# Optimization experiments

Hardware: AMD Instinct MI355X
Metric: run time of the kernel (lower is better)

## Reference

```python
import jax, jax.numpy as jnp
import numpy as np

D_MODEL = 1024
N_HEADS = 16
HEAD_DIM = D_MODEL // N_HEADS
NUM_MEM = 32
D_FF = 4 * D_MODEL
EPS = 1e-5


def _layer_norm(x, g, b):
    mu = jnp.mean(x, axis=-1, keepdims=True)
    var = jnp.mean(jnp.square(x - mu), axis=-1, keepdims=True)
    return (x - mu) * jax.lax.rsqrt(var + EPS) * g + b


def setup_inputs() -> dict:
    key = jax.random.key(0)
    ks = jax.random.split(key, 16)
    E, F, M = D_MODEL, D_FF, NUM_MEM
    s = 1.0 / np.sqrt(E)
    inp = {
        "src": jax.random.normal(ks[0], (2048, 2, E), dtype=jnp.float32),
        "in_proj_w": jax.random.uniform(ks[1], (3 * E, E), jnp.float32, -s, s),
        "in_proj_b": jnp.zeros((3 * E,), jnp.float32),
        "out_w": jax.random.uniform(ks[2], (E, E), jnp.float32, -s, s),
        "out_b": jnp.zeros((E,), jnp.float32),
        "mem_k": jax.random.normal(ks[3], (M, 1, E), jnp.float32) * (1.0 / HEAD_DIM),
        "mem_v": jax.random.normal(ks[4], (M, 1, E), jnp.float32) * (1.0 / M),
        "w1": jax.random.uniform(ks[5], (F, E), jnp.float32, -s, s),
        "b1": jnp.zeros((F,), jnp.float32),
        "w2": jax.random.uniform(ks[6], (E, F), jnp.float32, -1.0 / np.sqrt(F), 1.0 / np.sqrt(F)),
        "b2": jnp.zeros((E,), jnp.float32),
        "ln1_g": jnp.ones((E,), jnp.float32),
        "ln1_b": jnp.zeros((E,), jnp.float32),
        "ln2_g": jnp.ones((E,), jnp.float32),
        "ln2_b": jnp.zeros((E,), jnp.float32),
    }
    return inp


def reference(src, in_proj_w, in_proj_b, out_w, out_b, mem_k, mem_v,
              w1, b1, w2, b2, ln1_g, ln1_b, ln2_g, ln2_b):
    T, B, E = src.shape
    H, d, M = N_HEADS, HEAD_DIM, NUM_MEM

    # --- self-attention with learned memory k/v tokens (dropout=0, eval) ---
    qkv = src @ in_proj_w.T + in_proj_b          # [T, B, 3E]
    q, k, v = jnp.split(qkv, 3, axis=-1)
    q = q * (d ** -0.5)

    # scaled memory tokens appended to K/V along the sequence axis
    mk = (d ** 0.5) * jnp.broadcast_to(mem_k, (M, B, E))
    mv = (M ** 0.5) * jnp.broadcast_to(mem_v, (M, B, E))
    k = jnp.concatenate([k, mk], axis=0)          # [T+M, B, E]
    v = jnp.concatenate([v, mv], axis=0)

    qh = q.reshape(T, B, H, d)
    kh = k.reshape(T + M, B, H, d)
    vh = v.reshape(T + M, B, H, d)

    scores = jnp.einsum('tbhd,sbhd->bhts', qh, kh)  # [B, H, T, T+M]
    attn = jax.nn.softmax(scores, axis=-1)
    ctx = jnp.einsum('bhts,sbhd->tbhd', attn, vh).reshape(T, B, E)
    attn_out = ctx @ out_w.T + out_b

    # --- residual + LN, FFN, residual + LN (post-norm, relu) ---
    x = _layer_norm(src + attn_out, ln1_g, ln1_b)
    ffn = jax.nn.relu(x @ w1.T + b1) @ w2.T + b2
    return _layer_norm(x + ffn, ln2_g, ln2_b)
```

## Files before the change

### kernel.cpp

```cpp
#include <hip/hip_runtime.h>
#include <hip/hip_bf16.h>
#include <cstdint>


using bf16 = __hip_bfloat16;
typedef __attribute__((ext_vector_type(8))) __bf16 bf16x8;
typedef __attribute__((ext_vector_type(4))) __bf16 bf16x4;
typedef __attribute__((ext_vector_type(4))) float f32x4;

__device__ __forceinline__ void gload_lds16(const void* g, void* l) {
    auto gp = (const __attribute__((address_space(1))) void*)(uintptr_t)g;
    auto lp = (__attribute__((address_space(3))) void*)(uint32_t)(uintptr_t)l;
    __builtin_amdgcn_global_load_lds(gp, lp, 16, 0, 0);
}

__device__ __forceinline__ float fast_exp2(float x) {
#if __has_builtin(__builtin_amdgcn_exp2f)
    return __builtin_amdgcn_exp2f(x);
#else
    float r;
    asm("v_exp_f32 %0, %1" : "=v"(r) : "v"(x));
    return r;
#endif
}

__device__ __forceinline__ bf16 bf16_rn(float x) {
    uint32_t u = __builtin_bit_cast(uint32_t, x);
    uint16_t h = (uint16_t)((u + 0x8000u) >> 16);
    return __builtin_bit_cast(bf16, h);
}

__device__ __forceinline__ float bf2f(__bf16 x) {
    return (float)x;
}

template <int EPI>
__global__ __launch_bounds__(256, 2) void gemm_bt(
    const bf16* __restrict__ A, const bf16* __restrict__ B,
    const float* __restrict__ bias, bf16* __restrict__ Cb,
    int M, int N, int K, int lda) {
    __shared__ alignas(16) bf16 As[128 * 32];
    __shared__ alignas(16) bf16 Bs[128 * 32];

    const int tid = threadIdx.x;
    const int wid = tid >> 6;
    const int lane = tid & 63;
    const int g = lane >> 4;
    const int li = lane & 15;

    if (EPI == 3) {
        const int zo = blockIdx.z * K;
        A += zo;
        B += zo;
    }

    int wg = blockIdx.y * gridDim.x + blockIdx.x;
    const int nwg = gridDim.x * gridDim.y;
    const int cpx = nwg >> 3;
    wg = (wg & 7) * cpx + (wg >> 3);
    const int bx = wg % (int)gridDim.x;
    const int by = wg / (int)gridDim.x;

    const int row0 = by * 128;
    const int col0 = bx * 128;
    const int wr = (wid >> 1) * 64;
    const int wc = (wid & 1) * 64;

    const int c0 = wid, c1 = wid + 4;
    const int srow = lane >> 2;
    const int scol = (lane & 3) * 8;

    const bf16* Ag0 = A + (size_t)(row0 + c0 * 16 + srow) * lda + scol;
    const bf16* Ag1 = A + (size_t)(row0 + c1 * 16 + srow) * lda + scol;
    const bf16* Bg0 = B + (size_t)(col0 + c0 * 16 + srow) * lda + scol;
    const bf16* Bg1 = B + (size_t)(col0 + c1 * 16 + srow) * lda + scol;

    bf16* lA0 = &As[c0 * 512];
    bf16* lA1 = &As[c1 * 512];
    bf16* lB0 = &Bs[c0 * 512];
    bf16* lB1 = &Bs[c1 * 512];

    f32x4 acc[4][4];
#pragma unroll
    for (int i = 0; i < 4; ++i)
#pragma unroll
        for (int j = 0; j < 4; ++j) acc[i][j] = (f32x4){0.f, 0.f, 0.f, 0.f};

    for (int k0 = 0; k0 < K; k0 += 32) {
        gload_lds16(Ag0 + k0, lA0);
        gload_lds16(Ag1 + k0, lA1);
        gload_lds16(Bg0 + k0, lB0);
        gload_lds16(Bg1 + k0, lB1);
        __syncthreads();

        bf16x8 af[4], bfr[4];
#pragma unroll
        for (int i = 0; i < 4; ++i) {
            af[i] = *(const bf16x8*)&As[(wr + i * 16 + li) * 32 + g * 8];
            bfr[i] = *(const bf16x8*)&Bs[(wc + i * 16 + li) * 32 + g * 8];
        }
#pragma unroll
        for (int i = 0; i < 4; ++i)
#pragma unroll
            for (int j = 0; j < 4; ++j)
                acc[i][j] = __builtin_amdgcn_mfma_f32_16x16x32_bf16(af[i], bfr[j], acc[i][j], 0, 0, 0);
        __syncthreads();
    }

#pragma unroll
    for (int i = 0; i < 4; ++i) {
#pragma unroll
        for (int j = 0; j < 4; ++j) {
            const int col = col0 + wc + j * 16 + li;
            const float bv = (EPI == 3 && blockIdx.z != 0) ? 0.f : bias[col];
#pragma unroll
            for (int r = 0; r < 4; ++r) {
                const int row = row0 + wr + i * 16 + g * 4 + r;
                const size_t idx = (size_t)row * N + col;
                float v = acc[i][j][r] + bv;
                if (EPI == 0) {
                    if (col < 1024) v *= 0.18033688011112042f;
                    Cb[idx] = bf16_rn(v);
                } else if (EPI == 2) {
                    Cb[idx] = bf16_rn(v > 0.f ? v : 0.f);
                } else {
                    Cb[(size_t)blockIdx.z * ((size_t)M * N) + idx] = bf16_rn(v);
                }
            }
        }
    }
}

__global__ __launch_bounds__(256) void transpose_v(const bf16* __restrict__ qkv,
                                                   const bf16* __restrict__ mv,
                                                   bf16* __restrict__ vt) {
    __shared__ bf16 tile[64][72];
    const int t = blockIdx.x;
    const int h = blockIdx.y;
    const int b = blockIdx.z;
    const int tid = threadIdx.x;
    const int r = tid >> 2;
    const int c = (tid & 3) * 16;
    const int s0 = t * 64;
    if (t < 32) {
        const bf16* p = qkv + (size_t)((s0 + r) * 2 + b) * 3072 + 2048 + h * 64 + c;
        *(bf16x8*)&tile[r][c] = *(const bf16x8*)p;
        *(bf16x8*)&tile[r][c + 8] = *(const bf16x8*)(p + 8);
    } else if (r < 32) {
        const bf16* p = mv + (size_t)r * 1024 + h * 64 + c;
        *(bf16x8*)&tile[r][c] = *(const bf16x8*)p;
        *(bf16x8*)&tile[r][c + 8] = *(const bf16x8*)(p + 8);
    }
    __syncthreads();
    const int d = tid >> 2;
    const int sc = (tid & 3) * 16;
    const int smax = (t < 32) ? 64 : 32;
    if (sc < smax) {
        bf16 tmp[16];
#pragma unroll
        for (int j = 0; j < 16; ++j) tmp[j] = tile[sc + j][d];
        bf16* q = vt + (size_t)((b * 16 + h) * 64 + d) * 2080 + s0 + sc;
        *(bf16x8*)q = *(const bf16x8*)&tmp[0];
        *(bf16x8*)(q + 8) = *(const bf16x8*)&tmp[8];
    }
}

__global__ __launch_bounds__(256, 2) void attn_kernel(
    const bf16* __restrict__ qkv, const bf16* __restrict__ mk,
    const bf16* __restrict__ vt, bf16* __restrict__ ctx) {
    __shared__ alignas(16) bf16 Kst[4][64 * 64];
    __shared__ alignas(16) bf16 Vst[4][64 * 64];
    __shared__ alignas(16) bf16 Plds[4][32 * 64];

    const int tid = threadIdx.x;
    const int wid = tid >> 6;
    const int lane = tid & 63;
    const int g = lane >> 4;
    const int li = lane & 15;

    const int h = blockIdx.x;
    const int b = blockIdx.z;
    const int q0 = blockIdx.y * 128 + wid * 32;

    bf16* pl = &Plds[wid][0];
    const bf16* vth = vt + (size_t)((b * 16 + h) * 64) * 2080;

    const int srow8 = lane >> 3;
    const int sslot = (lane & 7) ^ srow8;

#define STAGE_KV(buf, t)                                                                       \
    {                                                                                          \
        const int _s0 = (t) * 64;                                                              \
        _Pragma("unroll") for (int j = 0; j < 2; ++j) {                                        \
            const int rw = (wid * 2 + j) * 8 + srow8;                                          \
            gload_lds16(qkv + (size_t)((_s0 + rw) * 2 + b) * 3072 + 1024 + h * 64 + sslot * 8, \
                        &Kst[buf][(wid * 2 + j) * 512]);                                       \
            gload_lds16(vth + (size_t)rw * 2080 + _s0 + sslot * 8,                             \
                        &Vst[buf][(wid * 2 + j) * 512]);                                       \
        }                                                                                      \
    }

    bf16x8 qf[2][2];
#pragma unroll
    for (int mi = 0; mi < 2; ++mi)
#pragma unroll
        for (int kd = 0; kd < 2; ++kd)
            qf[mi][kd] = *(const bf16x8*)(qkv + (size_t)((q0 + mi * 16 + li) * 2 + b) * 3072 +
                                          h * 64 + kd * 32 + g * 8);

    f32x4 o[2][4];
    float lrow[2][4];
#pragma unroll
    for (int mi = 0; mi < 2; ++mi) {
#pragma unroll
        for (int ni = 0; ni < 4; ++ni) o[mi][ni] = (f32x4){0.f, 0.f, 0.f, 0.f};
#pragma unroll
        for (int r = 0; r < 4; ++r) lrow[mi][r] = 0.f;
    }

    STAGE_KV(0, 0);
    STAGE_KV(1, 1);

    for (int tp = 0; tp < 16; ++tp) {
        const int t0 = tp * 2;
        __syncthreads();
        if (t0 + 2 < 32) STAGE_KV((t0 + 2) & 3, t0 + 2);
        if (t0 + 3 < 32) STAGE_KV((t0 + 3) & 3, t0 + 3);

#pragma unroll
        for (int ti = 0; ti < 2; ++ti) {
            const int t = t0 + ti;
            const int cur = t & 3;

            bf16x8 kf[4][2];
#pragma unroll
            for (int si = 0; si < 4; ++si)
#pragma unroll
                for (int kd = 0; kd < 2; ++kd)
                    kf[si][kd] = *(const bf16x8*)&Kst[cur][(si * 16 + li) * 64 +
                                                           (((kd * 4 + g) ^ (li & 7)) * 8)];

            f32x4 sa[2][4];
#pragma unroll
            for (int mi = 0; mi < 2; ++mi)
#pragma unroll
                for (int si = 0; si < 4; ++si) sa[mi][si] = (f32x4){0.f, 0.f, 0.f, 0.f};
            __builtin_amdgcn_s_setprio(1);
#pragma unroll
            for (int mi = 0; mi < 2; ++mi)
#pragma unroll
                for (int si = 0; si < 4; ++si)
#pragma unroll
                    for (int kd = 0; kd < 2; ++kd)
                        sa[mi][si] = __builtin_amdgcn_mfma_f32_16x16x32_bf16(qf[mi][kd], kf[si][kd],
                                                                             sa[mi][si], 0, 0, 0);
            __builtin_amdgcn_s_setprio(0);

            bf16x8 vf[2][4];
#pragma unroll
            for (int sblk = 0; sblk < 2; ++sblk)
#pragma unroll
                for (int ni = 0; ni < 4; ++ni)
                    vf[sblk][ni] = *(const bf16x8*)&Vst[cur][(ni * 16 + li) * 64 +
                                                             (((sblk * 4 + g) ^ (li & 7)) * 8)];

#pragma unroll
            for (int mi = 0; mi < 2; ++mi)
#pragma unroll
                for (int r = 0; r < 4; ++r) {
                    float ps = 0.f;
#pragma unroll
                    for (int si = 0; si < 4; ++si) {
                        const float p = fast_exp2(sa[mi][si][r]);
                        sa[mi][si][r] = p;
                        ps += p;
                    }
                    lrow[mi][r] += ps;
                }

#pragma unroll
            for (int mi = 0; mi < 2; ++mi)
#pragma unroll
                for (int si = 0; si < 4; ++si)
#pragma unroll
                    for (int r = 0; r < 4; ++r) {
                        const int row = mi * 16 + g * 4 + r;
                        const int col = (si * 16 + li) ^ (((row >> 2) & 3) << 4);
                        pl[row * 64 + col] = bf16_rn(sa[mi][si][r]);
                    }

            asm volatile("s_waitcnt lgkmcnt(0)" ::: "memory");
            __builtin_amdgcn_sched_barrier(0);

            bf16x8 pa[2][2];
#pragma unroll
            for (int mi = 0; mi < 2; ++mi)
#pragma unroll
                for (int sblk = 0; sblk < 2; ++sblk) {
                    const int row = mi * 16 + li;
                    const int e = (sblk * 32 + g * 8) ^ (((row >> 2) & 3) << 4);
                    pa[mi][sblk] = *(const bf16x8*)&pl[row * 64 + e];
                }

            __builtin_amdgcn_s_setprio(1);
#pragma unroll
            for (int sblk = 0; sblk < 2; ++sblk)
#pragma unroll
                for (int ni = 0; ni < 4; ++ni)
#pragma unroll
                    for (int mi = 0; mi < 2; ++mi)
                        o[mi][ni] = __builtin_amdgcn_mfma_f32_16x16x32_bf16(
                            pa[mi][sblk], vf[sblk][ni], o[mi][ni], 0, 0, 0);
            __builtin_amdgcn_s_setprio(0);
        }
    }

    {
        bf16x8 kf[2][2];
#pragma unroll
        for (int si = 0; si < 2; ++si)
#pragma unroll
            for (int kd = 0; kd < 2; ++kd)
                kf[si][kd] = *(const bf16x8*)(mk + (size_t)(si * 16 + li) * 1024 + h * 64 +
                                              kd * 32 + g * 8);
        bf16x8 vf[4];
#pragma unroll
        for (int ni = 0; ni < 4; ++ni)
            vf[ni] = *(const bf16x8*)(vth + (size_t)(ni * 16 + li) * 2080 + 2048 + g * 8);

        f32x4 sa[2][2];
#pragma unroll
        for (int mi = 0; mi < 2; ++mi)
#pragma unroll
            for (int si = 0; si < 2; ++si) sa[mi][si] = (f32x4){0.f, 0.f, 0.f, 0.f};
#pragma unroll
        for (int mi = 0; mi < 2; ++mi)
#pragma unroll
            for (int si = 0; si < 2; ++si)
#pragma unroll
                for (int kd = 0; kd < 2; ++kd)
                    sa[mi][si] = __builtin_amdgcn_mfma_f32_16x16x32_bf16(qf[mi][kd], kf[si][kd],
                                                                         sa[mi][si], 0, 0, 0);
#pragma unroll
        for (int mi = 0; mi < 2; ++mi)
#pragma unroll
            for (int r = 0; r < 4; ++r) {
                float ps = 0.f;
#pragma unroll
                for (int si = 0; si < 2; ++si) {
                    const float p = fast_exp2(sa[mi][si][r]);
                    sa[mi][si][r] = p;
                    ps += p;
                }
                lrow[mi][r] += ps;
            }
#pragma unroll
        for (int mi = 0; mi < 2; ++mi)
#pragma unroll
            for (int si = 0; si < 2; ++si)
#pragma unroll
                for (int r = 0; r < 4; ++r) {
                    const int row = mi * 16 + g * 4 + r;
                    const int col = (si * 16 + li) ^ (((row >> 2) & 3) << 4);
                    pl[row * 64 + col] = bf16_rn(sa[mi][si][r]);
                }

        asm volatile("s_waitcnt lgkmcnt(0)" ::: "memory");
        __builtin_amdgcn_sched_barrier(0);

        bf16x8 pa[2];
#pragma unroll
        for (int mi = 0; mi < 2; ++mi) {
            const int row = mi * 16 + li;
            const int e = (g * 8) ^ (((row >> 2) & 3) << 4);
            pa[mi] = *(const bf16x8*)&pl[row * 64 + e];
        }
#pragma unroll
        for (int ni = 0; ni < 4; ++ni)
#pragma unroll
            for (int mi = 0; mi < 2; ++mi)
                o[mi][ni] = __builtin_amdgcn_mfma_f32_16x16x32_bf16(pa[mi], vf[ni], o[mi][ni], 0, 0, 0);
    }

#pragma unroll
    for (int mi = 0; mi < 2; ++mi)
#pragma unroll
        for (int r = 0; r < 4; ++r) {
            float s = lrow[mi][r];
#pragma unroll
            for (int d = 1; d < 16; d <<= 1) s += __shfl_xor(s, d);
            const float inv = 1.f / s;
            const int trow = q0 + mi * 16 + g * 4 + r;
#pragma unroll
            for (int ni = 0; ni < 4; ++ni)
                ctx[(size_t)(trow * 2 + b) * 1024 + h * 64 + ni * 16 + li] =
                    bf16_rn(o[mi][ni][r] * inv);
        }
#undef STAGE_KV
}

__global__ __launch_bounds__(256, 4) void ln_sum_kernel(
    const bf16* __restrict__ pbase, const float* __restrict__ resf,
    const bf16* __restrict__ resb, const float* __restrict__ gw, const float* __restrict__ bw,
    float* __restrict__ y, bf16* __restrict__ ybf) {
    const int row = blockIdx.x;
    const int tid = threadIdx.x;
    const size_t base = (size_t)row * 1024 + tid * 4;
    const size_t PS = (size_t)4096 * 1024;

    float4 v = {0.f, 0.f, 0.f, 0.f};
#pragma unroll
    for (int z = 0; z < 4; ++z) {
        const bf16x4 a = *(const bf16x4*)(pbase + z * PS + base);
        v.x += bf2f(a[0]);
        v.y += bf2f(a[1]);
        v.z += bf2f(a[2]);
        v.w += bf2f(a[3]);
    }
    if (resf) {
        const float4 xr = ((const float4*)(resf + (size_t)row * 1024))[tid];
        v.x += xr.x; v.y += xr.y; v.z += xr.z; v.w += xr.w;
    } else {
        const bf16x4 xr = *(const bf16x4*)(resb + base);
        v.x += bf2f(xr[0]); v.y += bf2f(xr[1]); v.z += bf2f(xr[2]); v.w += bf2f(xr[3]);
    }

    float s = v.x + v.y + v.z + v.w;
    float s2 = v.x * v.x + v.y * v.y + v.z * v.z + v.w * v.w;
#pragma unroll
    for (int d = 1; d < 64; d <<= 1) {
        s += __shfl_xor(s, d);
        s2 += __shfl_xor(s2, d);
    }
    __shared__ float red[8];
    const int wid = tid >> 6, lane = tid & 63;
    if (lane == 0) { red[wid] = s; red[4 + wid] = s2; }
    __syncthreads();
    s = red[0] + red[1] + red[2] + red[3];
    s2 = red[4] + red[5] + red[6] + red[7];
    const float mu = s * (1.f / 1024.f);
    const float var = s2 * (1.f / 1024.f) - mu * mu;
    const float rstd = rsqrtf(var + 1e-5f);
    const float4 gv = ((const float4*)gw)[tid];
    const float4 bv = ((const float4*)bw)[tid];
    float4 out;
    out.x = (v.x - mu) * rstd * gv.x + bv.x;
    out.y = (v.y - mu) * rstd * gv.y + bv.y;
    out.z = (v.z - mu) * rstd * gv.z + bv.z;
    out.w = (v.w - mu) * rstd * gv.w + bv.w;
    if (y) ((float4*)(y + (size_t)row * 1024))[tid] = out;
    if (ybf) {
        bf16* yb = ybf + base;
        yb[0] = bf16_rn(out.x);
        yb[1] = bf16_rn(out.y);
        yb[2] = bf16_rn(out.z);
        yb[3] = bf16_rn(out.w);
    }
}

__global__ void cvt_all_kernel(const float* __restrict__ s0, const float* __restrict__ s1,
                               const float* __restrict__ s2, const float* __restrict__ s3,
                               const float* __restrict__ s4, const float* __restrict__ s5,
                               const float* __restrict__ s6, bf16* __restrict__ d0,
                               bf16* __restrict__ d1, bf16* __restrict__ d2, bf16* __restrict__ d3,
                               bf16* __restrict__ d4, bf16* __restrict__ d5, bf16* __restrict__ d6) {
    int i = blockIdx.x * 256 + threadIdx.x;
    const float* in;
    bf16* out;
    float scale = 1.f;
    if (i < 1048576) {
        in = s0; out = d0;
    } else if (i < 1835008) {
        in = s1; out = d1; i -= 1048576;
    } else if (i < 2097152) {
        in = s2; out = d2; i -= 1835008;
    } else if (i < 3145728) {
        in = s3; out = d3; i -= 2097152;
    } else if (i < 4194304) {
        in = s4; out = d4; i -= 3145728;
    } else if (i < 4202496) {
        in = s5; out = d5; i -= 4194304; scale = 8.f;
    } else {
        in = s6; out = d6; i -= 4202496; scale = 5.656854249492381f;
    }
    const float4 v = ((const float4*)in)[i];
    bf16* op = out + (size_t)i * 4;
    op[0] = bf16_rn(v.x * scale);
    op[1] = bf16_rn(v.y * scale);
    op[2] = bf16_rn(v.z * scale);
    op[3] = bf16_rn(v.w * scale);
}

extern "C" void kernel_launch(void* const* d_in, const int* in_sizes, int n_in, void* d_out,
                              int out_size, void* d_ws, size_t ws_size, hipStream_t stream) {
    const float* src = (const float*)d_in[0];
    const float* inproj_w = (const float*)d_in[1];
    const float* inproj_b = (const float*)d_in[2];
    const float* outw = (const float*)d_in[3];
    const float* outb = (const float*)d_in[4];
    const float* memk = (const float*)d_in[5];
    const float* memv = (const float*)d_in[6];
    const float* w1 = (const float*)d_in[7];
    const float* b1 = (const float*)d_in[8];
    const float* w2 = (const float*)d_in[9];
    const float* b2 = (const float*)d_in[10];
    const float* ln1g = (const float*)d_in[11];
    const float* ln1b = (const float*)d_in[12];
    const float* ln2g = (const float*)d_in[13];
    const float* ln2b = (const float*)d_in[14];

    char* ws = (char*)d_ws;
    const size_t MB = 1024 * 1024;
    bf16* w_inproj_bf = (bf16*)(ws + 0);
    bf16* w_out_bf = (bf16*)(ws + 6 * MB);
    bf16* w1_bf = (bf16*)(ws + 8 * MB);
    bf16* w2_bf = (bf16*)(ws + 16 * MB);
    bf16* mk_bf = (bf16*)(ws + 24 * MB);
    bf16* mv_bf = (bf16*)(ws + 24 * MB + 65536);
    bf16* src_bf = (bf16*)(ws + 25 * MB);
    bf16* ctx_bf = src_bf;
    bf16* x_bf = src_bf;
    bf16* qkv_bf = (bf16*)(ws + 33 * MB);
    bf16* g2p = qkv_bf;
    bf16* h_bf = qkv_bf;
    bf16* vt_bf = (bf16*)(ws + 65 * MB);
    bf16* g4p = vt_bf;
    float* outp = (float*)d_out;

    cvt_all_kernel<<<dim3(16448), dim3(256), 0, stream>>>(
        src, inproj_w, outw, w1, w2, memk, memv,
        src_bf, w_inproj_bf, w_out_bf, w1_bf, w2_bf, mk_bf, mv_bf);

    gemm_bt<0><<<dim3(3072 / 128, 4096 / 128), 256, 0, stream>>>(
        src_bf, w_inproj_bf, inproj_b, qkv_bf, 4096, 3072, 1024, 1024);
    transpose_v<<<dim3(33, 16, 2), 256, 0, stream>>>(qkv_bf, mv_bf, vt_bf);
    attn_kernel<<<dim3(16, 16, 2), 256, 0, stream>>>(qkv_bf, mk_bf, vt_bf, ctx_bf);
    gemm_bt<3><<<dim3(1024 / 128, 4096 / 128, 4), 256, 0, stream>>>(
        ctx_bf, w_out_bf, outb, g2p, 4096, 1024, 256, 1024);
    ln_sum_kernel<<<dim3(4096), 256, 0, stream>>>(g2p, src, nullptr, ln1g, ln1b, nullptr, x_bf);
    gemm_bt<2><<<dim3(4096 / 128, 4096 / 128), 256, 0, stream>>>(
        x_bf, w1_bf, b1, h_bf, 4096, 4096, 1024, 1024);
    gemm_bt<3><<<dim3(1024 / 128, 4096 / 128, 4), 256, 0, stream>>>(
        h_bf, w2_bf, b2, g4p, 4096, 1024, 1024, 4096);
    ln_sum_kernel<<<dim3(4096), 256, 0, stream>>>(g4p, nullptr, x_bf, ln2g, ln2b, outp, nullptr);
}
```

Measured before the change: 231.8 us.

## Switch attention to 32x32 MFMA with transposed scores and register-resident P

Rewrites the attention inner loop to use 32x32x16 bf16 MFMA, computing S^T (keys × queries) so each lane holds one query column. The probabilities are packed to bf16 with v_cvt_pk_bf16_f32 and reshuffled into A-operand layout with v_permlane32_swap, removing the per-wave LDS round-trip for P along with its waitcnt and sched barrier. The row-sum normalization is reworked to use cross-half shuffles. This trades LDS traffic for register permutes and relies on exact MFMA lane-layout assumptions, so any layout mistake would break correctness.

```diff
diff --git a/kernel.cpp b/kernel.cpp
--- a/kernel.cpp
+++ b/kernel.cpp
@@ -7,6 +7,7 @@
 typedef __attribute__((ext_vector_type(8))) __bf16 bf16x8;
 typedef __attribute__((ext_vector_type(4))) __bf16 bf16x4;
 typedef __attribute__((ext_vector_type(4))) float f32x4;
+typedef __attribute__((ext_vector_type(16))) float f32x16;
 
 __device__ __forceinline__ void gload_lds16(const void* g, void* l) {
     auto gp = (const __attribute__((address_space(1))) void*)(uintptr_t)g;
@@ -32,6 +33,16 @@
 
 __device__ __forceinline__ float bf2f(__bf16 x) {
     return (float)x;
+}
+
+__device__ __forceinline__ unsigned cvt_pk_bf16(float a, float b) {
+    unsigned r;
+    asm("v_cvt_pk_bf16_f32 %0, %1, %2" : "=v"(r) : "v"(a), "v"(b));
+    return r;
+}
+
+__device__ __forceinline__ void pl32swap(unsigned& a, unsigned& b) {
+    asm volatile("v_permlane32_swap_b32 %0, %1" : "+v"(a), "+v"(b));
 }
 
 template <int EPI>
@@ -170,19 +181,18 @@
     const bf16* __restrict__ vt, bf16* __restrict__ ctx) {
     __shared__ alignas(16) bf16 Kst[4][64 * 64];
     __shared__ alignas(16) bf16 Vst[4][64 * 64];
-    __shared__ alignas(16) bf16 Plds[4][32 * 64];
 
     const int tid = threadIdx.x;
     const int wid = tid >> 6;
     const int lane = tid & 63;
-    const int g = lane >> 4;
-    const int li = lane & 15;
+    const int l31 = lane & 31;
+    const int hh = lane >> 5;
+    const int l7 = lane & 7;
 
     const int h = blockIdx.x;
     const int b = blockIdx.z;
     const int q0 = blockIdx.y * 128 + wid * 32;
 
-    bf16* pl = &Plds[wid][0];
     const bf16* vth = vt + (size_t)((b * 16 + h) * 64) * 2080;
 
     const int srow8 = lane >> 3;
@@ -200,23 +210,20 @@
         }                                                                                      \
     }
 
-    bf16x8 qf[2][2];
-#pragma unroll
-    for (int mi = 0; mi < 2; ++mi)
-#pragma unroll
-        for (int kd = 0; kd < 2; ++kd)
-            qf[mi][kd] = *(const bf16x8*)(qkv + (size_t)((q0 + mi * 16 + li) * 2 + b) * 3072 +
-                                          h * 64 + kd * 32 + g * 8);
-
-    f32x4 o[2][4];
-    float lrow[2][4];
-#pragma unroll
-    for (int mi = 0; mi < 2; ++mi) {
-#pragma unroll
-        for (int ni = 0; ni < 4; ++ni) o[mi][ni] = (f32x4){0.f, 0.f, 0.f, 0.f};
-#pragma unroll
-        for (int r = 0; r < 4; ++r) lrow[mi][r] = 0.f;
-    }
+    bf16x8 qf[4];
+#pragma unroll
+    for (int dc = 0; dc < 4; ++dc)
+        qf[dc] = *(const bf16x8*)(qkv + (size_t)((q0 + l31) * 2 + b) * 3072 + h * 64 + dc * 16 +
+                                  hh * 8);
+
+    f32x16 zero16;
+#pragma unroll
+    for (int i = 0; i < 16; ++i) zero16[i] = 0.f;
+
+    f32x16 o[2];
+    o[0] = zero16;
+    o[1] = zero16;
+    float lrow = 0.f;
 
     STAGE_KV(0, 0);
     STAGE_KV(1, 1);
@@ -229,173 +236,116 @@
 
 #pragma unroll
         for (int ti = 0; ti < 2; ++ti) {
-            const int t = t0 + ti;
-            const int cur = t & 3;
-
-            bf16x8 kf[4][2];
-#pragma unroll
-            for (int si = 0; si < 4; ++si)
-#pragma unroll
-                for (int kd = 0; kd < 2; ++kd)
-                    kf[si][kd] = *(const bf16x8*)&Kst[cur][(si * 16 + li) * 64 +
-                                                           (((kd * 4 + g) ^ (li & 7)) * 8)];
-
-            f32x4 sa[2][4];
-#pragma unroll
-            for (int mi = 0; mi < 2; ++mi)
-#pragma unroll
-                for (int si = 0; si < 4; ++si) sa[mi][si] = (f32x4){0.f, 0.f, 0.f, 0.f};
+            const int cur = (t0 + ti) & 3;
+            const bf16* kbase = &Kst[cur][0];
+            const bf16* vbase = &Vst[cur][0];
+
+            f32x16 sa[2];
+            sa[0] = zero16;
+            sa[1] = zero16;
             __builtin_amdgcn_s_setprio(1);
 #pragma unroll
-            for (int mi = 0; mi < 2; ++mi)
-#pragma unroll
-                for (int si = 0; si < 4; ++si)
-#pragma unroll
-                    for (int kd = 0; kd < 2; ++kd)
-                        sa[mi][si] = __builtin_amdgcn_mfma_f32_16x16x32_bf16(qf[mi][kd], kf[si][kd],
-                                                                             sa[mi][si], 0, 0, 0);
+            for (int dc = 0; dc < 4; ++dc)
+#pragma unroll
+                for (int kb = 0; kb < 2; ++kb) {
+                    const int row = kb * 32 + l31;
+                    const bf16x8 ka =
+                        *(const bf16x8*)&kbase[row * 64 + (((dc * 2 + hh) ^ l7) * 8)];
+                    sa[kb] = __builtin_amdgcn_mfma_f32_32x32x16_bf16(ka, qf[dc], sa[kb], 0, 0, 0);
+                }
             __builtin_amdgcn_s_setprio(0);
 
-            bf16x8 vf[2][4];
-#pragma unroll
-            for (int sblk = 0; sblk < 2; ++sblk)
-#pragma unroll
-                for (int ni = 0; ni < 4; ++ni)
-                    vf[sblk][ni] = *(const bf16x8*)&Vst[cur][(ni * 16 + li) * 64 +
-                                                             (((sblk * 4 + g) ^ (li & 7)) * 8)];
-
-#pragma unroll
-            for (int mi = 0; mi < 2; ++mi)
-#pragma unroll
-                for (int r = 0; r < 4; ++r) {
-                    float ps = 0.f;
-#pragma unroll
-                    for (int si = 0; si < 4; ++si) {
-                        const float p = fast_exp2(sa[mi][si][r]);
-                        sa[mi][si][r] = p;
-                        ps += p;
-                    }
-                    lrow[mi][r] += ps;
+            unsigned pk[2][8];
+#pragma unroll
+            for (int kb = 0; kb < 2; ++kb)
+#pragma unroll
+                for (int m = 0; m < 8; ++m) {
+                    const float p0 = fast_exp2(sa[kb][2 * m]);
+                    const float p1 = fast_exp2(sa[kb][2 * m + 1]);
+                    lrow += p0 + p1;
+                    pk[kb][m] = cvt_pk_bf16(p0, p1);
                 }
 
-#pragma unroll
-            for (int mi = 0; mi < 2; ++mi)
-#pragma unroll
-                for (int si = 0; si < 4; ++si)
-#pragma unroll
-                    for (int r = 0; r < 4; ++r) {
-                        const int row = mi * 16 + g * 4 + r;
-                        const int col = (si * 16 + li) ^ (((row >> 2) & 3) << 4);
-                        pl[row * 64 + col] = bf16_rn(sa[mi][si][r]);
-                    }
-
-            asm volatile("s_waitcnt lgkmcnt(0)" ::: "memory");
-            __builtin_amdgcn_sched_barrier(0);
-
-            bf16x8 pa[2][2];
-#pragma unroll
-            for (int mi = 0; mi < 2; ++mi)
-#pragma unroll
-                for (int sblk = 0; sblk < 2; ++sblk) {
-                    const int row = mi * 16 + li;
-                    const int e = (sblk * 32 + g * 8) ^ (((row >> 2) & 3) << 4);
-                    pa[mi][sblk] = *(const bf16x8*)&pl[row * 64 + e];
+            __builtin_amdgcn_s_setprio(1);
+#pragma unroll
+            for (int kc = 0; kc < 4; ++kc) {
+                const int kb = kc >> 1;
+                const int base = (kc & 1) * 4;
+                unsigned A0 = pk[kb][base], A1 = pk[kb][base + 2];
+                unsigned B0 = pk[kb][base + 1], B1 = pk[kb][base + 3];
+                pl32swap(A0, A1);
+                pl32swap(B0, B1);
+                union {
+                    unsigned u[4];
+                    bf16x8 v;
+                } pa;
+                pa.u[0] = A0;
+                pa.u[1] = B0;
+                pa.u[2] = A1;
+                pa.u[3] = B1;
+#pragma unroll
+                for (int dt = 0; dt < 2; ++dt) {
+                    const int row = dt * 32 + l31;
+                    const bf16x8 vb =
+                        *(const bf16x8*)&vbase[row * 64 + (((kc * 2 + hh) ^ l7) * 8)];
+                    o[dt] = __builtin_amdgcn_mfma_f32_32x32x16_bf16(pa.v, vb, o[dt], 0, 0, 0);
                 }
-
-            __builtin_amdgcn_s_setprio(1);
-#pragma unroll
-            for (int sblk = 0; sblk < 2; ++sblk)
-#pragma unroll
-                for (int ni = 0; ni < 4; ++ni)
-#pragma unroll
-                    for (int mi = 0; mi < 2; ++mi)
-                        o[mi][ni] = __builtin_amdgcn_mfma_f32_16x16x32_bf16(
-                            pa[mi][sblk], vf[sblk][ni], o[mi][ni], 0, 0, 0);
+            }
             __builtin_amdgcn_s_setprio(0);
         }
     }
 
     {
-        bf16x8 kf[2][2];
-#pragma unroll
-        for (int si = 0; si < 2; ++si)
-#pragma unroll
-            for (int kd = 0; kd < 2; ++kd)
-                kf[si][kd] = *(const bf16x8*)(mk + (size_t)(si * 16 + li) * 1024 + h * 64 +
-                                              kd * 32 + g * 8);
-        bf16x8 vf[4];
-#pragma unroll
-        for (int ni = 0; ni < 4; ++ni)
-            vf[ni] = *(const bf16x8*)(vth + (size_t)(ni * 16 + li) * 2080 + 2048 + g * 8);
-
-        f32x4 sa[2][2];
-#pragma unroll
-        for (int mi = 0; mi < 2; ++mi)
-#pragma unroll
-            for (int si = 0; si < 2; ++si) sa[mi][si] = (f32x4){0.f, 0.f, 0.f, 0.f};
-#pragma unroll
-        for (int mi = 0; mi < 2; ++mi)
-#pragma unroll
-            for (int si = 0; si < 2; ++si)
-#pragma unroll
-                for (int kd = 0; kd < 2; ++kd)
-                    sa[mi][si] = __builtin_amdgcn_mfma_f32_16x16x32_bf16(qf[mi][kd], kf[si][kd],
-                                                                         sa[mi][si], 0, 0, 0);
-#pragma unroll
-        for (int mi = 0; mi < 2; ++mi)
-#pragma unroll
-            for (int r = 0; r < 4; ++r) {
-                float ps = 0.f;
-#pragma unroll
-                for (int si = 0; si < 2; ++si) {
-                    const float p = fast_exp2(sa[mi][si][r]);
-                    sa[mi][si][r] = p;
-                    ps += p;
-                }
-                lrow[mi][r] += ps;
+        f32x16 sat = zero16;
+#pragma unroll
+        for (int dc = 0; dc < 4; ++dc) {
+            const bf16x8 ka =
+                *(const bf16x8*)(mk + (size_t)l31 * 1024 + h * 64 + dc * 16 + hh * 8);
+            sat = __builtin_amdgcn_mfma_f32_32x32x16_bf16(ka, qf[dc], sat, 0, 0, 0);
+        }
+        unsigned pkt[8];
+#pragma unroll
+        for (int m = 0; m < 8; ++m) {
+            const float p0 = fast_exp2(sat[2 * m]);
+            const float p1 = fast_exp2(sat[2 * m + 1]);
+            lrow += p0 + p1;
+            pkt[m] = cvt_pk_bf16(p0, p1);
+        }
+#pragma unroll
+        for (int kc = 0; kc < 2; ++kc) {
+            const int base = kc * 4;
+            unsigned A0 = pkt[base], A1 = pkt[base + 2];
+            unsigned B0 = pkt[base + 1], B1 = pkt[base + 3];
+            pl32swap(A0, A1);
+            pl32swap(B0, B1);
+            union {
+                unsigned u[4];
+                bf16x8 v;
+            } pa;
+            pa.u[0] = A0;
+            pa.u[1] = B0;
+            pa.u[2] = A1;
+            pa.u[3] = B1;
+#pragma unroll
+            for (int dt = 0; dt < 2; ++dt) {
+                const bf16x8 vb = *(const bf16x8*)(vth + (size_t)(dt * 32 + l31) * 2080 + 2048 +
+                                                   kc * 16 + hh * 8);
+                o[dt] = __builtin_amdgcn_mfma_f32_32x32x16_bf16(pa.v, vb, o[dt], 0, 0, 0);
             }
-#pragma unroll
-        for (int mi = 0; mi < 2; ++mi)
-#pragma unroll
-            for (int si = 0; si < 2; ++si)
-#pragma unroll
-                for (int r = 0; r < 4; ++r) {
-                    const int row = mi * 16 + g * 4 + r;
-                    const int col = (si * 16 + li) ^ (((row >> 2) & 3) << 4);
-                    pl[row * 64 + col] = bf16_rn(sa[mi][si][r]);
-                }
-
-        asm volatile("s_waitcnt lgkmcnt(0)" ::: "memory");
-        __builtin_amdgcn_sched_barrier(0);
-
-        bf16x8 pa[2];
-#pragma unroll
-        for (int mi = 0; mi < 2; ++mi) {
-            const int row = mi * 16 + li;
-            const int e = (g * 8) ^ (((row >> 2) & 3) << 4);
-            pa[mi] = *(const bf16x8*)&pl[row * 64 + e];
-        }
-#pragma unroll
-        for (int ni = 0; ni < 4; ++ni)
-#pragma unroll
-            for (int mi = 0; mi < 2; ++mi)
-                o[mi][ni] = __builtin_amdgcn_mfma_f32_16x16x32_bf16(pa[mi], vf[ni], o[mi][ni], 0, 0, 0);
-    }
-
-#pragma unroll
-    for (int mi = 0; mi < 2; ++mi)
-#pragma unroll
-        for (int r = 0; r < 4; ++r) {
-            float s = lrow[mi][r];
-#pragma unroll
-            for (int d = 1; d < 16; d <<= 1) s += __shfl_xor(s, d);
-            const float inv = 1.f / s;
-            const int trow = q0 + mi * 16 + g * 4 + r;
-#pragma unroll
-            for (int ni = 0; ni < 4; ++ni)
-                ctx[(size_t)(trow * 2 + b) * 1024 + h * 64 + ni * 16 + li] =
-                    bf16_rn(o[mi][ni][r] * inv);
-        }
+        }
+    }
+
+    const float ssum = lrow + __shfl_xor(lrow, 32);
+    const float inv_own = 1.f / ssum;
+#pragma unroll
+    for (int r = 0; r < 16; ++r) {
+        const int qr = (r & 3) + 8 * (r >> 2) + 4 * hh;
+        const float iv = __shfl(inv_own, qr);
+#pragma unroll
+        for (int dt = 0; dt < 2; ++dt)
+            ctx[(size_t)((q0 + qr) * 2 + b) * 1024 + h * 64 + dt * 32 + l31] =
+                bf16_rn(o[dt][r] * iv);
+    }
 #undef STAGE_KV
 }
 
```

Result: faster. 225.8 us (-2.6%).
